# Kernel optimization log

Hardware: AMD Instinct MI355X
Metric: run time of the kernel (lower is better)

The kernel has to match this reference:

```python
import jax, jax.numpy as jnp
import numpy as np

BS = 4
N_NODES = 10000
N_FEAT = 64
HID = 128
N_LAYERS = 4
HID_FC = 512
N_CLASSES = 10
N_EDGES = 160000


def setup_inputs() -> dict:
    key = jax.random.key(0)
    ks = jax.random.split(key, 10)
    x = jax.random.normal(ks[0], (BS, N_NODES, N_FEAT), jnp.float32)
    edge_index = jax.random.randint(ks[1], (2, N_EDGES), 0, N_NODES, dtype=jnp.int32)
    # batch[b*N_NODES + i] = b, matching x.view(num_nodes*bs, -1) row-major flatten
    batch = jnp.repeat(jnp.arange(BS, dtype=jnp.int32), N_NODES)
    W1 = jax.random.normal(ks[2], (N_FEAT, HID), jnp.float32) * (N_FEAT ** -0.5)
    b1 = jax.random.normal(ks[3], (HID,), jnp.float32) * 0.01
    Ws = jax.random.normal(ks[4], (N_LAYERS - 1, HID, HID), jnp.float32) * (HID ** -0.5)
    bconvs = jax.random.normal(ks[5], (N_LAYERS - 1, HID), jnp.float32) * 0.01
    lin1_w = jax.random.normal(ks[6], (N_LAYERS * HID, HID_FC), jnp.float32) * ((N_LAYERS * HID) ** -0.5)
    lin1_b = jax.random.normal(ks[7], (HID_FC,), jnp.float32) * 0.01
    lin2_w = jax.random.normal(ks[8], (HID_FC, N_CLASSES), jnp.float32) * (HID_FC ** -0.5)
    lin2_b = jax.random.normal(ks[9], (N_CLASSES,), jnp.float32) * 0.01
    return {"x": x, "edge_index": edge_index, "batch": batch,
            "W1": W1, "b1": b1, "Ws": Ws, "bconvs": bconvs,
            "lin1_w": lin1_w, "lin1_b": lin1_b, "lin2_w": lin2_w, "lin2_b": lin2_b}


def _gcn_norm(edge_index, n):
    # PyG GCNConv: add self-loops, symmetric normalization D^-1/2 (A+I) D^-1/2
    loops = jnp.arange(n, dtype=edge_index.dtype)
    src = jnp.concatenate([edge_index[0], loops])
    dst = jnp.concatenate([edge_index[1], loops])
    deg = jnp.zeros((n,), jnp.float32).at[dst].add(1.0)
    dinv = jnp.where(deg > 0, jax.lax.rsqrt(deg), 0.0)
    return src, dst, dinv[src] * dinv[dst]


def reference(x, edge_index, batch, W1, b1, Ws, bconvs, lin1_w, lin1_b, lin2_w, lin2_b):
    bs, n, _ = x.shape
    src, dst, norm = _gcn_norm(edge_index, n)

    def gcn(h, W, b):
        m = (h @ W)[:, src, :] * norm[None, :, None]          # [bs, E+n, H]
        agg = jax.vmap(lambda mm: jax.ops.segment_sum(mm, dst, num_segments=n))(m)
        return agg + b

    h = jax.nn.relu(gcn(x, W1, b1))
    xs = [h]
    for i in range(Ws.shape[0]):
        h = jax.nn.relu(gcn(h, Ws[i], bconvs[i]))
        xs.append(h)
    # torch.stack(xs, -1).view(bs, n, -1): per-channel layer interleave
    h = jnp.stack(xs, -1).reshape(bs, n, -1)                   # [bs, n, L*H]
    flat = h.reshape(bs * n, -1)
    summed = jax.ops.segment_sum(flat, batch, num_segments=bs)
    counts = jax.ops.segment_sum(jnp.ones((bs * n,), flat.dtype), batch, num_segments=bs)
    pooled = summed / counts[:, None]                          # global_mean_pool
    h = jax.nn.relu(pooled @ lin1_w + lin1_b)
    # dropout p=0.5 is inference-disabled (training=False)
    logits = h @ lin2_w + lin2_b
    return jax.nn.log_softmax(logits, axis=-1)
```

## Files before the change

### kernel.cpp

```cpp
#include <hip/hip_runtime.h>
#include <hip/hip_bf16.h>
#include <math.h>

#define N_NODES 10000
#define N_EDGES 160000
#define BS      4
#define N_TOT   (BS * N_NODES)
#define HID     128
#define NPC     4
#define CHUNKS  (N_NODES/NPC)
#define HID_FC  512
#define N_CLASSES 10
#define N_LAYERS  4
#define DEG_CAP 64
#define ZERO_INT4 325000

using bf16x8 = __attribute__((ext_vector_type(8))) short;
using f32x4  = __attribute__((ext_vector_type(4))) float;
using f32x2  = __attribute__((ext_vector_type(2))) float;

__device__ __forceinline__ unsigned bf_rne(float x) {
    unsigned b = __float_as_uint(x);
    return (b + 0x7fffu + ((b >> 16) & 1u)) >> 16;
}
__device__ __forceinline__ float bf2f(unsigned hi16) { return __uint_as_float(hi16 << 16); }

#if __has_builtin(__builtin_amdgcn_cvt_pk_f32_fp8) && __has_builtin(__builtin_amdgcn_cvt_pk_fp8_f32)
#define HW_FP8 1
#else
#define HW_FP8 0
#endif

__device__ __forceinline__ float fp8_dec1(unsigned b) {
    unsigned s = (b & 0x80u) << 24;
    unsigned em = b & 0x7Fu;
    float mag;
    if (em >= 8u) mag = __uint_as_float((((em >> 3) + 120u) << 23) | ((em & 7u) << 20));
    else          mag = (float)em * 0x1p-9f;
    return __uint_as_float(s | __float_as_uint(mag));
}

__device__ __forceinline__ unsigned fp8_enc(float x) {
#if HW_FP8
    return (unsigned)(__builtin_amdgcn_cvt_pk_fp8_f32(x, x, 0, false) & 0xFF);
#else
    unsigned s = (__float_as_uint(x) >> 24) & 0x80u;
    float ax = fabsf(x);
    unsigned r;
    if (ax >= 0x1p-6f) {
        if (ax > 448.f) r = 0x7Eu;
        else {
            unsigned b = __float_as_uint(ax);
            unsigned t = b + 0x7FFFFu + ((b >> 20) & 1u);
            r = (t >> 20) - 960u;
        }
    } else {
        r = (unsigned)__float2int_rn(ax * 512.f);
    }
    return s | r;
#endif
}

__device__ __forceinline__ void fp8x8_dec(uint2 u, float* f) {
#if HW_FP8
    f32x2 p0 = __builtin_amdgcn_cvt_pk_f32_fp8((int)u.x, false);
    f32x2 p1 = __builtin_amdgcn_cvt_pk_f32_fp8((int)u.x, true);
    f32x2 p2 = __builtin_amdgcn_cvt_pk_f32_fp8((int)u.y, false);
    f32x2 p3 = __builtin_amdgcn_cvt_pk_f32_fp8((int)u.y, true);
    f[0] = p0[0]; f[1] = p0[1]; f[2] = p1[0]; f[3] = p1[1];
    f[4] = p2[0]; f[5] = p2[1]; f[6] = p3[0]; f[7] = p3[1];
#else
    f[0] = fp8_dec1(u.x & 0xFFu);         f[1] = fp8_dec1((u.x >> 8) & 0xFFu);
    f[2] = fp8_dec1((u.x >> 16) & 0xFFu); f[3] = fp8_dec1((u.x >> 24) & 0xFFu);
    f[4] = fp8_dec1(u.y & 0xFFu);         f[5] = fp8_dec1((u.y >> 8) & 0xFFu);
    f[6] = fp8_dec1((u.y >> 16) & 0xFFu); f[7] = fp8_dec1((u.y >> 24) & 0xFFu);
#endif
}

__global__ __launch_bounds__(256) void k_prep(const float* __restrict__ x,
                                              const float* __restrict__ W1,
                                              const float* __restrict__ Ws,
                                              int4* __restrict__ zbase,
                                              ushort* __restrict__ x_bf,
                                              ushort* __restrict__ wt_hi,
                                              ushort* __restrict__ wt_lo) {
    const int gt = blockIdx.x * 256 + threadIdx.x, NT = gridDim.x * 256;
    for (int i = gt; i < ZERO_INT4; i += NT) zbase[i] = make_int4(0, 0, 0, 0);
    for (int i = gt; i < 640000; i += NT) {
        float4 v = ((const float4*)x)[i];
        ushort4 o;
        o.x = (ushort)bf_rne(v.x); o.y = (ushort)bf_rne(v.y);
        o.z = (ushort)bf_rne(v.z); o.w = (ushort)bf_rne(v.w);
        ((ushort4*)x_bf)[i] = o;
    }
    for (int i = gt; i < 57344; i += NT) {
        float v;
        if (i < 8192) { int c = i >> 6, k = i & 63; v = W1[k * HID + c]; }
        else {
            int tt = i - 8192, li = tt >> 14, rem = tt & 16383;
            int c = rem >> 7, k = rem & 127;
            v = Ws[li * 16384 + k * HID + c];
        }
        unsigned hi = bf_rne(v);
        unsigned lo = bf_rne(v - bf2f(hi));
        wt_hi[i] = (ushort)hi;
        wt_lo[i] = (ushort)lo;
    }
}

__global__ void k_count(const int* __restrict__ ei, int* __restrict__ counts) {
    int e = blockIdx.x * 256 + threadIdx.x;
    if (e < N_EDGES) atomicAdd(&counts[ei[N_EDGES + e]], 1);
}

__global__ void k_fill(const int* __restrict__ ei, const int* __restrict__ counts,
                       int* __restrict__ cursor, int2* __restrict__ csr) {
    int e = blockIdx.x * 256 + threadIdx.x;
    if (e < N_EDGES) {
        int s = ei[e], d = ei[N_EDGES + e];
        float ws = rsqrtf((float)(counts[s] + 1));
        int pos = atomicAdd(&cursor[d], 1);
        if (pos < DEG_CAP)
            csr[(d << 6) + pos] = make_int2(s, __float_as_int(ws));
    }
}

template<int K>
__global__ __launch_bounds__(256) void k_mm(const ushort* __restrict__ A,
                                            const ushort* __restrict__ Bt_hi,
                                            const ushort* __restrict__ Bt_lo,
                                            unsigned char* __restrict__ outF8) {
    constexpr int NS = K / 32;
    const int lane = threadIdx.x & 63;
    const int w    = threadIdx.x >> 6;
    const int row_base = blockIdx.x * 128 + w * 32;
    const int lr = lane & 15, lg = lane >> 4;

    bf16x8 a[2][NS];
    #pragma unroll
    for (int rh = 0; rh < 2; ++rh) {
        int r = row_base + rh * 16 + lr;
        if (r > N_TOT - 1) r = N_TOT - 1;
        const ushort* ap = A + (size_t)r * K + lg * 8;
        #pragma unroll
        for (int s = 0; s < NS; ++s)
            a[rh][s] = *(const bf16x8*)(ap + s * 32);
    }

    f32x4 acc[2][8];
    #pragma unroll
    for (int rh = 0; rh < 2; ++rh)
        #pragma unroll
        for (int n = 0; n < 8; ++n)
            acc[rh][n] = (f32x4){0.f, 0.f, 0.f, 0.f};

    #pragma unroll
    for (int n = 0; n < 8; ++n) {
        const ushort* bp = Bt_hi + (size_t)(n * 16 + lr) * K + lg * 8;
        const ushort* bq = Bt_lo + (size_t)(n * 16 + lr) * K + lg * 8;
        #pragma unroll
        for (int s = 0; s < NS; ++s) {
            bf16x8 bh = *(const bf16x8*)(bp + s * 32);
            bf16x8 bl = *(const bf16x8*)(bq + s * 32);
            acc[0][n] = __builtin_amdgcn_mfma_f32_16x16x32_bf16(a[0][s], bh, acc[0][n], 0, 0, 0);
            acc[1][n] = __builtin_amdgcn_mfma_f32_16x16x32_bf16(a[1][s], bh, acc[1][n], 0, 0, 0);
            acc[0][n] = __builtin_amdgcn_mfma_f32_16x16x32_bf16(a[0][s], bl, acc[0][n], 0, 0, 0);
            acc[1][n] = __builtin_amdgcn_mfma_f32_16x16x32_bf16(a[1][s], bl, acc[1][n], 0, 0, 0);
        }
    }

    #pragma unroll
    for (int rh = 0; rh < 2; ++rh) {
        int rb = row_base + rh * 16 + lg * 4;
        #pragma unroll
        for (int n = 0; n < 8; ++n) {
            int col = n * 16 + lr;
            #pragma unroll
            for (int j = 0; j < 4; ++j) {
                int r = rb + j;
                if (r < N_TOT) {
                    int b = r / N_NODES;
                    int nd = r - b * N_NODES;
                    outF8[(size_t)nd * 512 + b * 128 + col] =
                        (unsigned char)fp8_enc(acc[rh][n][j]);
                }
            }
        }
    }
}

__global__ __launch_bounds__(128) void k_agg(const uint2* __restrict__ tmp8,
                                             const int* __restrict__ counts,
                                             const int2* __restrict__ csr,
                                             const float* __restrict__ bias,
                                             uint4* __restrict__ hA,
                                             float* __restrict__ partial) {
    const int chunk = blockIdx.x;
    const int w = threadIdx.x >> 6, l = threadIdx.x & 63;
    const int b = l >> 4, c0 = (l & 15) * 8;
    float bvv[8];
    {
        float4 b0 = *(const float4*)(bias + c0);
        float4 b1 = *(const float4*)(bias + c0 + 4);
        bvv[0] = b0.x; bvv[1] = b0.y; bvv[2] = b0.z; bvv[3] = b0.w;
        bvv[4] = b1.x; bvv[5] = b1.y; bvv[6] = b1.z; bvv[7] = b1.w;
    }
    float pool[8];
    #pragma unroll
    for (int j = 0; j < 8; ++j) pool[j] = 0.f;

    const int n0 = chunk * NPC + w * (NPC / 2);
    for (int n = n0; n < n0 + NPC / 2; ++n) {
        int cnt = counts[n];
        const float dn = rsqrtf((float)(cnt + 1));
        if (cnt > DEG_CAP) cnt = DEG_CAP;
        const int no = (cnt + 7) >> 3;
        float acc[8];
        {
            uint2 us = tmp8[n * 64 + l];
            float sf[8];
            fp8x8_dec(us, sf);
            #pragma unroll
            for (int j = 0; j < 8; ++j) acc[j] = dn * sf[j];
        }
        const int4* cp = (const int4*)(csr + ((size_t)n << 6));
        for (int q = 0; q < no; ++q) {
            int4 q0 = cp[4 * q], q1 = cp[4 * q + 1], q2 = cp[4 * q + 2], q3 = cp[4 * q + 3];
            uint2 u0 = tmp8[q0.x * 64 + l];
            uint2 u1 = tmp8[q0.z * 64 + l];
            uint2 u2 = tmp8[q1.x * 64 + l];
            uint2 u3 = tmp8[q1.z * 64 + l];
            uint2 u4 = tmp8[q2.x * 64 + l];
            uint2 u5 = tmp8[q2.z * 64 + l];
            uint2 u6 = tmp8[q3.x * 64 + l];
            uint2 u7 = tmp8[q3.z * 64 + l];
            float w0 = __int_as_float(q0.y), w1 = __int_as_float(q0.w);
            float w2 = __int_as_float(q1.y), w3 = __int_as_float(q1.w);
            float w4 = __int_as_float(q2.y), w5 = __int_as_float(q2.w);
            float w6 = __int_as_float(q3.y), w7 = __int_as_float(q3.w);
            float f[8];
            fp8x8_dec(u0, f);
            #pragma unroll
            for (int j = 0; j < 8; ++j) acc[j] = fmaf(w0, f[j], acc[j]);
            fp8x8_dec(u1, f);
            #pragma unroll
            for (int j = 0; j < 8; ++j) acc[j] = fmaf(w1, f[j], acc[j]);
            fp8x8_dec(u2, f);
            #pragma unroll
            for (int j = 0; j < 8; ++j) acc[j] = fmaf(w2, f[j], acc[j]);
            fp8x8_dec(u3, f);
            #pragma unroll
            for (int j = 0; j < 8; ++j) acc[j] = fmaf(w3, f[j], acc[j]);
            fp8x8_dec(u4, f);
            #pragma unroll
            for (int j = 0; j < 8; ++j) acc[j] = fmaf(w4, f[j], acc[j]);
            fp8x8_dec(u5, f);
            #pragma unroll
            for (int j = 0; j < 8; ++j) acc[j] = fmaf(w5, f[j], acc[j]);
            fp8x8_dec(u6, f);
            #pragma unroll
            for (int j = 0; j < 8; ++j) acc[j] = fmaf(w6, f[j], acc[j]);
            fp8x8_dec(u7, f);
            #pragma unroll
            for (int j = 0; j < 8; ++j) acc[j] = fmaf(w7, f[j], acc[j]);
        }
        float r[8];
        #pragma unroll
        for (int j = 0; j < 8; ++j) {
            r[j] = fmaxf(fmaf(dn, acc[j], bvv[j]), 0.f);
            pool[j] += r[j];
        }
        uint4 ov;
        ov.x = bf_rne(r[0]) | (bf_rne(r[1]) << 16);
        ov.y = bf_rne(r[2]) | (bf_rne(r[3]) << 16);
        ov.z = bf_rne(r[4]) | (bf_rne(r[5]) << 16);
        ov.w = bf_rne(r[6]) | (bf_rne(r[7]) << 16);
        hA[(size_t)(b * N_NODES + n) * 16 + (c0 >> 3)] = ov;
    }

    __shared__ float pw[64][8];
    if (w == 1) {
        #pragma unroll
        for (int j = 0; j < 8; ++j) pw[l][j] = pool[j];
    }
    __syncthreads();
    if (w == 0) {
        #pragma unroll
        for (int j = 0; j < 8; ++j) pool[j] += pw[l][j];
        float* pp = partial + ((size_t)b * CHUNKS + chunk) * HID + c0;
        *(float4*)pp = make_float4(pool[0], pool[1], pool[2], pool[3]);
        *(float4*)(pp + 4) = make_float4(pool[4], pool[5], pool[6], pool[7]);
    }
}

__global__ __launch_bounds__(512) void k_reduce(const float* __restrict__ partial,
                                                float* __restrict__ pooled) {
    const int lb = blockIdx.x;
    const int c = threadIdx.x & 127, qh = threadIdx.x >> 7;
    const float* p = partial + (size_t)lb * CHUNKS * HID + c;
    float s = 0.f;
    const int e0 = qh * (CHUNKS / 4), e1 = e0 + CHUNKS / 4;
    #pragma unroll 8
    for (int ch = e0; ch < e1; ++ch) s += p[(size_t)ch * HID];
    __shared__ float sm[4][128];
    sm[qh][c] = s;
    __syncthreads();
    if (qh == 0)
        pooled[(size_t)lb * HID + c] =
            (sm[0][c] + sm[1][c] + sm[2][c] + sm[3][c]) * (1.0f / N_NODES);
}

__global__ __launch_bounds__(256) void k_lin1(const float* __restrict__ pooled,
                                              const float* __restrict__ w,
                                              const float* __restrict__ bias,
                                              float* __restrict__ h1) {
    __shared__ float pf[BS][HID_FC];
    __shared__ float red[8][32][BS];
    const int t = threadIdx.x;
    const int o0 = blockIdx.x * 32;
    for (int i = t; i < BS * HID_FC; i += 256) {
        int b = i >> 9, f = i & 511;
        int l = f & 3, cc = f >> 2;
        pf[b][f] = pooled[(size_t)(l * BS + b) * HID + cc];
    }
    __syncthreads();
    const int o = t & 31, kq = t >> 5;
    float acc[BS] = {0.f, 0.f, 0.f, 0.f};
    #pragma unroll 4
    for (int k = kq * 64; k < kq * 64 + 64; ++k) {
        float wv = w[(size_t)k * HID_FC + o0 + o];
        #pragma unroll
        for (int b = 0; b < BS; ++b) acc[b] = fmaf(pf[b][k], wv, acc[b]);
    }
    #pragma unroll
    for (int b = 0; b < BS; ++b) red[kq][o][b] = acc[b];
    __syncthreads();
    if (t < 128) {
        int oo = t & 31, b = t >> 5;
        float s = 0.f;
        #pragma unroll
        for (int q = 0; q < 8; ++q) s += red[q][oo][b];
        s += bias[o0 + oo];
        h1[(size_t)b * HID_FC + o0 + oo] = fmaxf(s, 0.f);
    }
}

__global__ __launch_bounds__(512) void k_lin2(const float* __restrict__ h1,
                                              const float* __restrict__ w,
                                              const float* __restrict__ bias,
                                              float* __restrict__ out) {
    const int k = threadIdx.x;
    const int lane = k & 63, wv_id = k >> 6;
    float wrow[N_CLASSES];
    #pragma unroll
    for (int c = 0; c < N_CLASSES; ++c) wrow[c] = w[k * N_CLASSES + c];
    float hv[BS];
    #pragma unroll
    for (int b = 0; b < BS; ++b) hv[b] = h1[b * HID_FC + k];
    float acc[BS][N_CLASSES];
    #pragma unroll
    for (int b = 0; b < BS; ++b)
        #pragma unroll
        for (int c = 0; c < N_CLASSES; ++c) acc[b][c] = hv[b] * wrow[c];
    #pragma unroll
    for (int off = 32; off >= 1; off >>= 1) {
        #pragma unroll
        for (int b = 0; b < BS; ++b)
            #pragma unroll
            for (int c = 0; c < N_CLASSES; ++c)
                acc[b][c] += __shfl_down(acc[b][c], off);
    }
    __shared__ float red[8][BS * N_CLASSES];
    if (lane == 0) {
        #pragma unroll
        for (int b = 0; b < BS; ++b)
            #pragma unroll
            for (int c = 0; c < N_CLASSES; ++c)
                red[wv_id][b * N_CLASSES + c] = acc[b][c];
    }
    __syncthreads();
    __shared__ float logits[BS][N_CLASSES];
    if (k < BS * N_CLASSES) {
        int b = k / N_CLASSES, c = k % N_CLASSES;
        float s = bias[c];
        #pragma unroll
        for (int q = 0; q < 8; ++q) s += red[q][k];
        logits[b][c] = s;
    }
    __syncthreads();
    if (k < BS) {
        float m = logits[k][0];
        for (int i = 1; i < N_CLASSES; ++i) m = fmaxf(m, logits[k][i]);
        float s = 0.f;
        for (int i = 0; i < N_CLASSES; ++i) s += expf(logits[k][i] - m);
        float lse = m + logf(s);
        for (int i = 0; i < N_CLASSES; ++i) out[k * N_CLASSES + i] = logits[k][i] - lse;
    }
}

extern "C" void kernel_launch(void* const* d_in, const int* in_sizes, int n_in,
                              void* d_out, int out_size, void* d_ws, size_t ws_size,
                              hipStream_t stream) {
    const float* x       = (const float*)d_in[0];
    const int*   ei      = (const int*)d_in[1];
    const float* W1      = (const float*)d_in[3];
    const float* b1      = (const float*)d_in[4];
    const float* Ws      = (const float*)d_in[5];
    const float* bconvs  = (const float*)d_in[6];
    const float* lin1_w  = (const float*)d_in[7];
    const float* lin1_b  = (const float*)d_in[8];
    const float* lin2_w  = (const float*)d_in[9];
    const float* lin2_b  = (const float*)d_in[10];
    float* out = (float*)d_out;

    char* base = (char*)d_ws;
    unsigned char* tmp8 = (unsigned char*)base; base += (size_t)N_NODES * 512;
    ushort* hA16   = (ushort*)base;    base += (size_t)N_TOT * HID * 2;
    ushort* x_bf   = (ushort*)base;    base += (size_t)N_TOT * 64 * 2;
    ushort* wt_hi  = (ushort*)base;    base += 57344 * 2;
    ushort* wt_lo  = (ushort*)base;    base += 57344 * 2;
    float*  partial= (float*)base;     base += (size_t)N_LAYERS * BS * CHUNKS * HID * 4;
    float*  pooled = (float*)base;     base += N_LAYERS * BS * HID * 4;
    float*  h1     = (float*)base;     base += BS * HID_FC * 4;
    int*    counts = (int*)base;       base += N_NODES * 4;
    int*    cursor = (int*)base;       base += N_NODES * 4;
    int2*   csr    = (int2*)base;

    const int GE = (N_EDGES + 255) / 256;

    k_prep<<<1024, 256, 0, stream>>>(x, W1, Ws, (int4*)counts, x_bf, wt_hi, wt_lo);
    k_count<<<GE, 256, 0, stream>>>(ei, counts);
    k_fill<<<GE, 256, 0, stream>>>(ei, counts, cursor, csr);

    const int agg_grid = CHUNKS;
    const int mm_grid = (N_TOT + 127) / 128;

    k_mm<64><<<mm_grid, 256, 0, stream>>>(x_bf, wt_hi, wt_lo, tmp8);
    k_agg<<<agg_grid, 128, 0, stream>>>((const uint2*)tmp8, counts, csr, b1,
                                        (uint4*)hA16, partial);
    for (int l = 1; l < N_LAYERS; ++l) {
        const ushort* whi = wt_hi + 8192 + (size_t)(l - 1) * 16384;
        const ushort* wlo = wt_lo + 8192 + (size_t)(l - 1) * 16384;
        const float* bl = bconvs + (size_t)(l - 1) * HID;
        k_mm<128><<<mm_grid, 256, 0, stream>>>(hA16, whi, wlo, tmp8);
        k_agg<<<agg_grid, 128, 0, stream>>>((const uint2*)tmp8, counts, csr, bl,
                                            (uint4*)hA16,
                                            partial + (size_t)l * BS * CHUNKS * HID);
    }

    k_reduce<<<N_LAYERS * BS, 512, 0, stream>>>(partial, pooled);
    k_lin1<<<HID_FC / 32, 256, 0, stream>>>(pooled, lin1_w, lin1_b, h1);
    k_lin2<<<1, 512, 0, stream>>>(h1, lin2_w, lin2_b, out);
}
```

Before: 263.0 us.

## Fuse aggregation with next layer's matmul and pool via atomics

```diff
diff --git a/kernel.cpp b/kernel.cpp
--- a/kernel.cpp
+++ b/kernel.cpp
@@ -13,7 +13,7 @@
 #define N_CLASSES 10
 #define N_LAYERS  4
 #define DEG_CAP 64
-#define ZERO_INT4 325000
+#define ZERO_INT4 341384
 
 using bf16x8 = __attribute__((ext_vector_type(8))) short;
 using f32x4  = __attribute__((ext_vector_type(4))) float;
@@ -75,6 +75,68 @@
     f[4] = fp8_dec1(u.y & 0xFFu);         f[5] = fp8_dec1((u.y >> 8) & 0xFFu);
     f[6] = fp8_dec1((u.y >> 16) & 0xFFu); f[7] = fp8_dec1((u.y >> 24) & 0xFFu);
 #endif
+}
+
+__device__ __forceinline__ void agg_node(const uint2* __restrict__ tin,
+                                         const int* __restrict__ counts,
+                                         const int2* __restrict__ csr,
+                                         int n, int l, const float* bvv, float* r) {
+    int cnt = counts[n];
+    const float dn = rsqrtf((float)(cnt + 1));
+    if (cnt > DEG_CAP) cnt = DEG_CAP;
+    const int no = (cnt + 7) >> 3;
+    float acc[8];
+    {
+        uint2 us = tin[n * 64 + l];
+        float sf[8];
+        fp8x8_dec(us, sf);
+        #pragma unroll
+        for (int j = 0; j < 8; ++j) acc[j] = dn * sf[j];
+    }
+    const int4* cp = (const int4*)(csr + ((size_t)n << 6));
+    for (int q = 0; q < no; ++q) {
+        int4 q0 = cp[4 * q], q1 = cp[4 * q + 1], q2 = cp[4 * q + 2], q3 = cp[4 * q + 3];
+        uint2 u0 = tin[q0.x * 64 + l];
+        uint2 u1 = tin[q0.z * 64 + l];
+        uint2 u2 = tin[q1.x * 64 + l];
+        uint2 u3 = tin[q1.z * 64 + l];
+        uint2 u4 = tin[q2.x * 64 + l];
+        uint2 u5 = tin[q2.z * 64 + l];
+        uint2 u6 = tin[q3.x * 64 + l];
+        uint2 u7 = tin[q3.z * 64 + l];
+        float w0 = __int_as_float(q0.y), w1 = __int_as_float(q0.w);
+        float w2 = __int_as_float(q1.y), w3 = __int_as_float(q1.w);
+        float w4 = __int_as_float(q2.y), w5 = __int_as_float(q2.w);
+        float w6 = __int_as_float(q3.y), w7 = __int_as_float(q3.w);
+        float f[8];
+        fp8x8_dec(u0, f);
+        #pragma unroll
+        for (int j = 0; j < 8; ++j) acc[j] = fmaf(w0, f[j], acc[j]);
+        fp8x8_dec(u1, f);
+        #pragma unroll
+        for (int j = 0; j < 8; ++j) acc[j] = fmaf(w1, f[j], acc[j]);
+        fp8x8_dec(u2, f);
+        #pragma unroll
+        for (int j = 0; j < 8; ++j) acc[j] = fmaf(w2, f[j], acc[j]);
+        fp8x8_dec(u3, f);
+        #pragma unroll
+        for (int j = 0; j < 8; ++j) acc[j] = fmaf(w3, f[j], acc[j]);
+        fp8x8_dec(u4, f);
+        #pragma unroll
+        for (int j = 0; j < 8; ++j) acc[j] = fmaf(w4, f[j], acc[j]);
+        fp8x8_dec(u5, f);
+        #pragma unroll
+        for (int j = 0; j < 8; ++j) acc[j] = fmaf(w5, f[j], acc[j]);
+        fp8x8_dec(u6, f);
+        #pragma unroll
+        for (int j = 0; j < 8; ++j) acc[j] = fmaf(w6, f[j], acc[j]);
+        fp8x8_dec(u7, f);
+        #pragma unroll
+        for (int j = 0; j < 8; ++j) acc[j] = fmaf(w7, f[j], acc[j]);
+    }
+    #pragma unroll
+    for (int j = 0; j < 8; ++j)
+        r[j] = fmaxf(fmaf(dn, acc[j], bvv[j]), 0.f);
 }
 
 __global__ __launch_bounds__(256) void k_prep(const float* __restrict__ x,
@@ -189,12 +251,114 @@
     }
 }
 
-__global__ __launch_bounds__(128) void k_agg(const uint2* __restrict__ tmp8,
-                                             const int* __restrict__ counts,
-                                             const int2* __restrict__ csr,
-                                             const float* __restrict__ bias,
-                                             uint4* __restrict__ hA,
-                                             float* __restrict__ partial) {
+__global__ __launch_bounds__(256) void k_fused_am(const uint2* __restrict__ tin,
+                                                  const int* __restrict__ counts,
+                                                  const int2* __restrict__ csr,
+                                                  const float* __restrict__ bias,
+                                                  const ushort* __restrict__ Bt_hi,
+                                                  const ushort* __restrict__ Bt_lo,
+                                                  unsigned char* __restrict__ tout,
+                                                  float* __restrict__ partial2) {
+    __shared__ ushort Al[64 * 128];
+    __shared__ float pw[4][64][8];
+    const int t = threadIdx.x;
+    const int w = t >> 6, l = t & 63;
+    const int b = l >> 4, ci = l & 15, c0 = ci * 8;
+    const int nd0 = blockIdx.x * 16;
+
+    float bvv[8];
+    {
+        float4 b0 = *(const float4*)(bias + c0);
+        float4 b1 = *(const float4*)(bias + c0 + 4);
+        bvv[0] = b0.x; bvv[1] = b0.y; bvv[2] = b0.z; bvv[3] = b0.w;
+        bvv[4] = b1.x; bvv[5] = b1.y; bvv[6] = b1.z; bvv[7] = b1.w;
+    }
+    float pool[8];
+    #pragma unroll
+    for (int j = 0; j < 8; ++j) pool[j] = 0.f;
+
+    for (int ni = 0; ni < 4; ++ni) {
+        const int n = nd0 + w * 4 + ni;
+        float r[8];
+        agg_node(tin, counts, csr, n, l, bvv, r);
+        #pragma unroll
+        for (int j = 0; j < 8; ++j) pool[j] += r[j];
+        const int row = ((w * 4 + ni) << 2) + b;
+        unsigned off = (unsigned)(row * 256 + ci * 16);
+        off ^= (unsigned)((row & 7) << 4);
+        uint4 ov;
+        ov.x = bf_rne(r[0]) | (bf_rne(r[1]) << 16);
+        ov.y = bf_rne(r[2]) | (bf_rne(r[3]) << 16);
+        ov.z = bf_rne(r[4]) | (bf_rne(r[5]) << 16);
+        ov.w = bf_rne(r[6]) | (bf_rne(r[7]) << 16);
+        *(uint4*)((char*)Al + off) = ov;
+    }
+    #pragma unroll
+    for (int j = 0; j < 8; ++j) pw[w][l][j] = pool[j];
+    __syncthreads();
+
+    if (w == 0) {
+        const int s = blockIdx.x & 31;
+        float* pp = partial2 + ((size_t)b * 32 + s) * HID + c0;
+        #pragma unroll
+        for (int j = 0; j < 8; ++j)
+            atomicAdd(&pp[j], pw[0][l][j] + pw[1][l][j] + pw[2][l][j] + pw[3][l][j]);
+    }
+
+    const int lr = l & 15, lg = l >> 4;
+    bf16x8 a[4];
+    {
+        const int row = w * 16 + lr;
+        const unsigned bx = (unsigned)(row * 256) ^ (unsigned)((row & 7) << 4);
+        #pragma unroll
+        for (int s = 0; s < 4; ++s)
+            a[s] = *(const bf16x8*)((const char*)Al + (bx ^ 0u) + ((lg * 16 + s * 64) ^ 0u)
+                                    - ((row * 256) & 0) + (((row * 256 + lg * 16 + s * 64)
+                                    ^ ((row & 7) << 4)) - (bx + lg * 16 + s * 64)) + lg * 16 + s * 64);
+    }
+    {
+        const int row = w * 16 + lr;
+        #pragma unroll
+        for (int s = 0; s < 4; ++s) {
+            unsigned off = (unsigned)(row * 256 + lg * 16 + s * 64);
+            off ^= (unsigned)((row & 7) << 4);
+            a[s] = *(const bf16x8*)((const char*)Al + off);
+        }
+    }
+
+    f32x4 acc[8];
+    #pragma unroll
+    for (int n = 0; n < 8; ++n) acc[n] = (f32x4){0.f, 0.f, 0.f, 0.f};
+    #pragma unroll
+    for (int n = 0; n < 8; ++n) {
+        const ushort* bp = Bt_hi + (size_t)(n * 16 + lr) * 128 + lg * 8;
+        const ushort* bq = Bt_lo + (size_t)(n * 16 + lr) * 128 + lg * 8;
+        #pragma unroll
+        for (int s = 0; s < 4; ++s) {
+            bf16x8 bh = *(const bf16x8*)(bp + s * 32);
+            bf16x8 bl = *(const bf16x8*)(bq + s * 32);
+            acc[n] = __builtin_amdgcn_mfma_f32_16x16x32_bf16(a[s], bh, acc[n], 0, 0, 0);
+            acc[n] = __builtin_amdgcn_mfma_f32_16x16x32_bf16(a[s], bl, acc[n], 0, 0, 0);
+        }
+    }
+
+    #pragma unroll
+    for (int n = 0; n < 8; ++n) {
+        const int col = n * 16 + lr;
+        #pragma unroll
+        for (int j = 0; j < 4; ++j) {
+            const int row = w * 16 + lg * 4 + j;
+            const int nd = nd0 + (row >> 2), bb = row & 3;
+            tout[(size_t)nd * 512 + bb * 128 + col] = (unsigned char)fp8_enc(acc[n][j]);
+        }
+    }
+}
+
+__global__ __launch_bounds__(128) void k_agg_last(const uint2* __restrict__ tin,
+                                                  const int* __restrict__ counts,
+                                                  const int2* __restrict__ csr,
+                                                  const float* __restrict__ bias,
+                                                  float* __restrict__ partial2) {
     const int chunk = blockIdx.x;
     const int w = threadIdx.x >> 6, l = threadIdx.x & 63;
     const int b = l >> 4, c0 = (l & 15) * 8;
@@ -208,76 +372,13 @@
     float pool[8];
     #pragma unroll
     for (int j = 0; j < 8; ++j) pool[j] = 0.f;
-
     const int n0 = chunk * NPC + w * (NPC / 2);
     for (int n = n0; n < n0 + NPC / 2; ++n) {
-        int cnt = counts[n];
-        const float dn = rsqrtf((float)(cnt + 1));
-        if (cnt > DEG_CAP) cnt = DEG_CAP;
-        const int no = (cnt + 7) >> 3;
-        float acc[8];
-        {
-            uint2 us = tmp8[n * 64 + l];
-            float sf[8];
-            fp8x8_dec(us, sf);
-            #pragma unroll
-            for (int j = 0; j < 8; ++j) acc[j] = dn * sf[j];
-        }
-        const int4* cp = (const int4*)(csr + ((size_t)n << 6));
-        for (int q = 0; q < no; ++q) {
-            int4 q0 = cp[4 * q], q1 = cp[4 * q + 1], q2 = cp[4 * q + 2], q3 = cp[4 * q + 3];
-            uint2 u0 = tmp8[q0.x * 64 + l];
-            uint2 u1 = tmp8[q0.z * 64 + l];
-            uint2 u2 = tmp8[q1.x * 64 + l];
-            uint2 u3 = tmp8[q1.z * 64 + l];
-            uint2 u4 = tmp8[q2.x * 64 + l];
-            uint2 u5 = tmp8[q2.z * 64 + l];
-            uint2 u6 = tmp8[q3.x * 64 + l];
-            uint2 u7 = tmp8[q3.z * 64 + l];
-            float w0 = __int_as_float(q0.y), w1 = __int_as_float(q0.w);
-            float w2 = __int_as_float(q1.y), w3 = __int_as_float(q1.w);
-            float w4 = __int_as_float(q2.y), w5 = __int_as_float(q2.w);
-            float w6 = __int_as_float(q3.y), w7 = __int_as_float(q3.w);
-            float f[8];
-            fp8x8_dec(u0, f);
-            #pragma unroll
-            for (int j = 0; j < 8; ++j) acc[j] = fmaf(w0, f[j], acc[j]);
-            fp8x8_dec(u1, f);
-            #pragma unroll
-            for (int j = 0; j < 8; ++j) acc[j] = fmaf(w1, f[j], acc[j]);
-            fp8x8_dec(u2, f);
-            #pragma unroll
-            for (int j = 0; j < 8; ++j) acc[j] = fmaf(w2, f[j], acc[j]);
-            fp8x8_dec(u3, f);
-            #pragma unroll
-            for (int j = 0; j < 8; ++j) acc[j] = fmaf(w3, f[j], acc[j]);
-            fp8x8_dec(u4, f);
-            #pragma unroll
-            for (int j = 0; j < 8; ++j) acc[j] = fmaf(w4, f[j], acc[j]);
-            fp8x8_dec(u5, f);
-            #pragma unroll
-            for (int j = 0; j < 8; ++j) acc[j] = fmaf(w5, f[j], acc[j]);
-            fp8x8_dec(u6, f);
-            #pragma unroll
-            for (int j = 0; j < 8; ++j) acc[j] = fmaf(w6, f[j], acc[j]);
-            fp8x8_dec(u7, f);
-            #pragma unroll
-            for (int j = 0; j < 8; ++j) acc[j] = fmaf(w7, f[j], acc[j]);
-        }
         float r[8];
-        #pragma unroll
-        for (int j = 0; j < 8; ++j) {
-            r[j] = fmaxf(fmaf(dn, acc[j], bvv[j]), 0.f);
-            pool[j] += r[j];
-        }
-        uint4 ov;
-        ov.x = bf_rne(r[0]) | (bf_rne(r[1]) << 16);
-        ov.y = bf_rne(r[2]) | (bf_rne(r[3]) << 16);
-        ov.z = bf_rne(r[4]) | (bf_rne(r[5]) << 16);
-        ov.w = bf_rne(r[6]) | (bf_rne(r[7]) << 16);
-        hA[(size_t)(b * N_NODES + n) * 16 + (c0 >> 3)] = ov;
-    }
-
+        agg_node(tin, counts, csr, n, l, bvv, r);
+        #pragma unroll
+        for (int j = 0; j < 8; ++j) pool[j] += r[j];
+    }
     __shared__ float pw[64][8];
     if (w == 1) {
         #pragma unroll
@@ -285,46 +386,38 @@
     }
     __syncthreads();
     if (w == 0) {
-        #pragma unroll
-        for (int j = 0; j < 8; ++j) pool[j] += pw[l][j];
-        float* pp = partial + ((size_t)b * CHUNKS + chunk) * HID + c0;
-        *(float4*)pp = make_float4(pool[0], pool[1], pool[2], pool[3]);
-        *(float4*)(pp + 4) = make_float4(pool[4], pool[5], pool[6], pool[7]);
-    }
-}
-
-__global__ __launch_bounds__(512) void k_reduce(const float* __restrict__ partial,
-                                                float* __restrict__ pooled) {
-    const int lb = blockIdx.x;
-    const int c = threadIdx.x & 127, qh = threadIdx.x >> 7;
-    const float* p = partial + (size_t)lb * CHUNKS * HID + c;
-    float s = 0.f;
-    const int e0 = qh * (CHUNKS / 4), e1 = e0 + CHUNKS / 4;
-    #pragma unroll 8
-    for (int ch = e0; ch < e1; ++ch) s += p[(size_t)ch * HID];
-    __shared__ float sm[4][128];
-    sm[qh][c] = s;
-    __syncthreads();
-    if (qh == 0)
-        pooled[(size_t)lb * HID + c] =
-            (sm[0][c] + sm[1][c] + sm[2][c] + sm[3][c]) * (1.0f / N_NODES);
-}
-
-__global__ __launch_bounds__(256) void k_lin1(const float* __restrict__ pooled,
+        const int s = chunk & 31;
+        float* pp = partial2 + ((size_t)(12 + b) * 32 + s) * HID + c0;
+        #pragma unroll
+        for (int j = 0; j < 8; ++j)
+            atomicAdd(&pp[j], pool[j] + pw[l][j]);
+    }
+}
+
+__global__ __launch_bounds__(256) void k_lin1(const float* __restrict__ partial2,
                                               const float* __restrict__ w,
                                               const float* __restrict__ bias,
                                               float* __restrict__ h1) {
+    __shared__ float pooled_s[16 * HID];
     __shared__ float pf[BS][HID_FC];
     __shared__ float red[8][32][BS];
     const int t = threadIdx.x;
-    const int o0 = blockIdx.x * 32;
+    for (int i = t; i < 16 * HID; i += 256) {
+        const float* p = partial2 + (size_t)(i >> 7) * 32 * HID + (i & 127);
+        float s = 0.f;
+        #pragma unroll
+        for (int q = 0; q < 32; ++q) s += p[q * HID];
+        pooled_s[i] = s * (1.0f / N_NODES);
+    }
+    __syncthreads();
     for (int i = t; i < BS * HID_FC; i += 256) {
         int b = i >> 9, f = i & 511;
-        int l = f & 3, cc = f >> 2;
-        pf[b][f] = pooled[(size_t)(l * BS + b) * HID + cc];
+        int ly = f & 3, cc = f >> 2;
+        pf[b][f] = pooled_s[(ly * 4 + b) * HID + cc];
     }
     __syncthreads();
     const int o = t & 31, kq = t >> 5;
+    const int o0 = blockIdx.x * 32;
     float acc[BS] = {0.f, 0.f, 0.f, 0.f};
     #pragma unroll 4
     for (int k = kq * 64; k < kq * 64 + 64; ++k) {
@@ -414,41 +507,41 @@
     float* out = (float*)d_out;
 
     char* base = (char*)d_ws;
-    unsigned char* tmp8 = (unsigned char*)base; base += (size_t)N_NODES * 512;
-    ushort* hA16   = (ushort*)base;    base += (size_t)N_TOT * HID * 2;
+    unsigned char* tmpA = (unsigned char*)base; base += (size_t)N_NODES * 512;
+    unsigned char* tmpB = (unsigned char*)base; base += (size_t)N_NODES * 512;
     ushort* x_bf   = (ushort*)base;    base += (size_t)N_TOT * 64 * 2;
     ushort* wt_hi  = (ushort*)base;    base += 57344 * 2;
     ushort* wt_lo  = (ushort*)base;    base += 57344 * 2;
-    float*  partial= (float*)base;     base += (size_t)N_LAYERS * BS * CHUNKS * HID * 4;
-    float*  pooled = (float*)base;     base += N_LAYERS * BS * HID * 4;
     float*  h1     = (float*)base;     base += BS * HID_FC * 4;
     int*    counts = (int*)base;       base += N_NODES * 4;
     int*    cursor = (int*)base;       base += N_NODES * 4;
-    int2*   csr    = (int2*)base;
+    int2*   csr    = (int2*)base;      base += (size_t)N_NODES * DEG_CAP * 8;
+    float*  partial2 = (float*)base;   base += (size_t)16 * 32 * HID * 4;
 
     const int GE = (N_EDGES + 255) / 256;
+    const int mm_grid = (N_TOT + 127) / 128;
 
     k_prep<<<1024, 256, 0, stream>>>(x, W1, Ws, (int4*)counts, x_bf, wt_hi, wt_lo);
     k_count<<<GE, 256, 0, stream>>>(ei, counts);
     k_fill<<<GE, 256, 0, stream>>>(ei, counts, cursor, csr);
 
-    const int agg_grid = CHUNKS;
-    const int mm_grid = (N_TOT + 127) / 128;
-
-    k_mm<64><<<mm_grid, 256, 0, stream>>>(x_bf, wt_hi, wt_lo, tmp8);
-    k_agg<<<agg_grid, 128, 0, stream>>>((const uint2*)tmp8, counts, csr, b1,
-                                        (uint4*)hA16, partial);
-    for (int l = 1; l < N_LAYERS; ++l) {
-        const ushort* whi = wt_hi + 8192 + (size_t)(l - 1) * 16384;
-        const ushort* wlo = wt_lo + 8192 + (size_t)(l - 1) * 16384;
-        const float* bl = bconvs + (size_t)(l - 1) * HID;
-        k_mm<128><<<mm_grid, 256, 0, stream>>>(hA16, whi, wlo, tmp8);
-        k_agg<<<agg_grid, 128, 0, stream>>>((const uint2*)tmp8, counts, csr, bl,
-                                            (uint4*)hA16,
-                                            partial + (size_t)l * BS * CHUNKS * HID);
-    }
-
-    k_reduce<<<N_LAYERS * BS, 512, 0, stream>>>(partial, pooled);
-    k_lin1<<<HID_FC / 32, 256, 0, stream>>>(pooled, lin1_w, lin1_b, h1);
+    k_mm<64><<<mm_grid, 256, 0, stream>>>(x_bf, wt_hi, wt_lo, tmpA);
+
+    unsigned char* tin = tmpA;
+    unsigned char* tou = tmpB;
+    for (int j = 0; j < 3; ++j) {
+        const float* bj = (j == 0) ? b1 : (bconvs + (size_t)(j - 1) * HID);
+        const ushort* whi = wt_hi + 8192 + (size_t)j * 16384;
+        const ushort* wlo = wt_lo + 8192 + (size_t)j * 16384;
+        k_fused_am<<<N_NODES / 16, 256, 0, stream>>>((const uint2*)tin, counts, csr, bj,
+                                                     whi, wlo, tou,
+                                                     partial2 + (size_t)j * 4 * 32 * HID);
+        unsigned char* tswap = tin; tin = tou; tou = tswap;
+    }
+
+    k_agg_last<<<CHUNKS, 128, 0, stream>>>((const uint2*)tin, counts, csr,
+                                           bconvs + 2 * HID, partial2);
+
+    k_lin1<<<HID_FC / 32, 256, 0, stream>>>(partial2, lin1_w, lin1_b, h1);
     k_lin2<<<1, 512, 0, stream>>>(h1, lin2_w, lin2_b, out);
 }
```

Result: faster. 237.7 us (-9.6%).
